# Optimization experiments

Measured on AMD Instinct MI355X. Metric: run time of the kernel, lower is better.

Reference implementation:

```python
import jax, jax.numpy as jnp
import numpy as np

GATE_SLOPE = 10.0
ALPHA = 0.8
STRIDE = 1
PADDING = 1


def _unfold(x, kH, kW, stride, padding):
    # torch F.unfold equivalent, kept as (B, Cin, kH, kW, Hout, Wout)
    B, C, H, W = x.shape
    xp = jnp.pad(x, ((0, 0), (0, 0), (padding, padding), (padding, padding)))
    Hout = (H + 2 * padding - kH) // stride + 1
    Wout = (W + 2 * padding - kW) // stride + 1
    cols = []
    for i in range(kH):          # small fixed loop over kernel taps (9 iters)
        for j in range(kW):
            cols.append(xp[:, :, i:i + Hout * stride:stride, j:j + Wout * stride:stride])
    return jnp.stack(cols, axis=2).reshape(B, C, kH, kW, Hout, Wout)


def setup_inputs() -> dict:
    key = jax.random.key(0)
    ks = jax.random.split(key, 6)
    B, Cin, H, W = 4, 16, 32, 32
    Cout, K, kH, kW = 32, 3, 3, 3
    pshape = (Cout, Cin, K, kH, kW)
    x = jax.random.normal(ks[0], (B, Cin, H, W), jnp.float32)
    k = jax.random.uniform(ks[1], pshape, jnp.float32) * 2.0 + 0.5
    Ec = jax.random.uniform(ks[2], pshape, jnp.float32) * 2.0 + 0.5
    Ps = jax.random.uniform(ks[3], pshape, jnp.float32) * 1.5 + 0.5
    bias = jax.random.normal(ks[4], pshape, jnp.float32) * 0.1
    coef = jax.random.normal(ks[5], pshape, jnp.float32)
    out_bias = jnp.zeros((Cout,), jnp.float32)
    return {"x": x, "k": k, "Ec": Ec, "Ps": Ps, "bias": bias, "coef": coef, "out_bias": out_bias}


def reference(x, k, Ec, Ps, bias, coef, out_bias):
    kH, kW = k.shape[-2], k.shape[-1]
    patches = _unfold(x, kH, kW, STRIDE, PADDING)          # (B,Cin,kH,kW,Hout,Wout)
    # broadcast layout: (B, Cout, Cin, K, kH, kW, Hout, Wout)
    xe = patches[:, None, :, None]                          # (B,1,Cin,1,kH,kW,Ho,Wo)
    def bc(p):
        return p[None, :, :, :, :, :, None, None]
    k_, Ec_, Ps_, b_, c_ = bc(k), bc(Ec), bc(Ps), bc(bias), bc(coef)
    # stateless mode: prev_x = detach(x_exp) -> dx == 0 in value, grad flows via xe
    prev_x = jax.lax.stop_gradient(xe)
    is_moving_up = jax.nn.sigmoid(GATE_SLOPE * (xe - prev_x))
    crossed_pos = jax.nn.sigmoid(GATE_SLOPE * (xe - Ec_))
    crossed_neg = jax.nn.sigmoid(GATE_SLOPE * (-xe - Ec_))
    su = is_moving_up * crossed_pos
    sl = (1.0 - is_moving_up) * crossed_neg
    # branch_prev = +1 (stateless)
    target_sign = su - sl + (1.0 - su - sl)
    branch_mom = ALPHA + (1.0 - ALPHA) * target_sign
    shifted_x = xe + Ec_ * branch_mom
    basis = Ps_ * jnp.tanh(k_ * shifted_x) + b_
    out = jnp.sum(basis * c_, axis=(2, 3, 4, 5))            # (B,Cout,Hout,Wout)
    return out + out_bias[None, :, None, None]
```

## Files before the change

kernel.cpp:

```cpp
#include <hip/hip_runtime.h>


#define LOG2E 1.4426950408889634f

__global__ __launch_bounds__(256, 8) void ferro_main(
    const float* __restrict__ x,
    const float* __restrict__ k, const float* __restrict__ Ec,
    const float* __restrict__ Ps, const float* __restrict__ bias,
    const float* __restrict__ coef, const float* __restrict__ out_bias,
    float* __restrict__ out)
{
    const int bid = blockIdx.x;
    const int rs  = bid & 15;
    const int co  = (bid >> 4) & 31;
    const int b   = bid >> 9;
    const int tid = threadIdx.x;

    __shared__ float4 p4s[432];
    __shared__ float  xs[16 * 4 * 34];
    __shared__ float  red[128];
    __shared__ float  redc[4];
    __shared__ float  csh;

    const int pbase = co * 432;
    float cpart = 0.f;
    for (int s = tid; s < 432; s += 256) {
        float kv = k[pbase + s];
        float ev = Ec[pbase + s];
        float pv = Ps[pbase + s];
        float bv = bias[pbase + s];
        float cv = coef[pbase + s];
        float G  = 2.f * LOG2E * kv;
        float4 v;
        v.x = ev;
        v.y = G;
        v.z = 0.1f * G * ev;
        v.w = -2.f * pv * cv;
        int cin = s / 27;
        int r   = s - cin * 27;
        int kk  = r / 9;
        int ij  = r - kk * 9;
        p4s[cin * 27 + ij * 3 + kk] = v;
        cpart += (pv + bv) * cv;
    }

    const int r0 = rs * 2;
    const float* xb = x + b * (16 * 1024);
    for (int idx = tid; idx < 16 * 136; idx += 256) {
        int cin  = idx / 136;
        int rem  = idx - cin * 136;
        int row4 = rem / 34;
        int colp = rem - row4 * 34;
        int gr = r0 + row4 - 1;
        int gc = colp - 1;
        float v = 0.f;
        if ((unsigned)gr < 32u && (unsigned)gc < 32u)
            v = xb[(cin * 32 + gr) * 32 + gc];
        xs[idx] = v;
    }

    #pragma unroll
    for (int off = 32; off > 0; off >>= 1)
        cpart += __shfl_down(cpart, off, 64);
    if ((tid & 63) == 0) redc[tid >> 6] = cpart;
    __syncthreads();
    if (tid == 0) csh = redc[0] + redc[1] + redc[2] + redc[3];
    __syncthreads();

    const int lane = tid & 63;
    const int w    = tid >> 6;
    const int row  = w >> 1;
    const int cinq = w & 1;
    const int col  = lane & 31;
    const int cinh = lane >> 5;
    float acc0 = 0.f, acc1 = 0.f, acc2 = 0.f;

    const int cinbase = cinq * 8 + cinh * 4;
    #pragma unroll 1
    for (int c = 0; c < 4; ++c) {
        const int cin = cinbase + c;
        const float*  xr = &xs[cin * 136 + row * 34 + col];
        const float4* pp = &p4s[cin * 27];
        #pragma unroll
        for (int ij = 0; ij < 9; ++ij) {
            const int i = ij / 3, j = ij - (ij / 3) * 3;
            float xv = xr[i * 34 + j];
            {
                float4 v = pp[ij * 3 + 0];
                float wv = xv + v.x;
                float q  = fmaf(wv, wv, 0.04f);
                float r  = __builtin_amdgcn_rsqf(q);
                float t  = fmaf(wv, r, -1.f);
                float a  = fmaf(v.z, t, v.y * wv);
                float e  = __builtin_amdgcn_exp2f(a);
                float u  = __builtin_amdgcn_rcpf(e + 1.f);
                acc0 = fmaf(v.w, u, acc0);
            }
            {
                float4 v = pp[ij * 3 + 1];
                float wv = xv + v.x;
                float q  = fmaf(wv, wv, 0.04f);
                float r  = __builtin_amdgcn_rsqf(q);
                float t  = fmaf(wv, r, -1.f);
                float a  = fmaf(v.z, t, v.y * wv);
                float e  = __builtin_amdgcn_exp2f(a);
                float u  = __builtin_amdgcn_rcpf(e + 1.f);
                acc1 = fmaf(v.w, u, acc1);
            }
            {
                float4 v = pp[ij * 3 + 2];
                float wv = xv + v.x;
                float q  = fmaf(wv, wv, 0.04f);
                float r  = __builtin_amdgcn_rsqf(q);
                float t  = fmaf(wv, r, -1.f);
                float a  = fmaf(v.z, t, v.y * wv);
                float e  = __builtin_amdgcn_exp2f(a);
                float u  = __builtin_amdgcn_rcpf(e + 1.f);
                acc2 = fmaf(v.w, u, acc2);
            }
        }
    }

    float acc = (acc0 + acc1) + acc2;
    acc += __shfl_xor(acc, 32, 64);
    if (cinh == 0) red[w * 32 + col] = acc;
    __syncthreads();

    if (tid < 64) {
        int r   = tid >> 5;
        int cl  = tid & 31;
        float v = red[(r * 2 + 0) * 32 + cl] + red[(r * 2 + 1) * 32 + cl]
                + csh + out_bias[co];
        out[((b * 32 + co) * 32 + (r0 + r)) * 32 + cl] = v;
    }
}

extern "C" void kernel_launch(void* const* d_in, const int* in_sizes, int n_in,
                              void* d_out, int out_size, void* d_ws, size_t ws_size,
                              hipStream_t stream) {
    const float* x        = (const float*)d_in[0];
    const float* k        = (const float*)d_in[1];
    const float* Ec       = (const float*)d_in[2];
    const float* Ps       = (const float*)d_in[3];
    const float* bias     = (const float*)d_in[4];
    const float* coef     = (const float*)d_in[5];
    const float* out_bias = (const float*)d_in[6];
    float* out = (float*)d_out;

    ferro_main<<<dim3(2048), dim3(256), 0, stream>>>(
        x, k, Ec, Ps, bias, coef, out_bias, out);
}
```

Measured before the change: 87.46 us.

## Split parameter prep into separate kernel and process four rows per block

Parameter preprocessing (the float4 packing and the constant bias term) moves into a small prep kernel that writes to workspace, so it is no longer repeated in every block of the main kernel. The main kernel then reads the parameters from global memory with wave-uniform indexing instead of from shared memory. Each block now covers four output rows instead of two, which halves the block count and reduces halo reloads of x. In exchange there is an extra kernel launch and a dependency between the two kernels, and the parameter reads now go through cache rather than LDS.

After: 91.42 us. 4.5% more time.

```diff
diff --git a/kernel.cpp b/kernel.cpp
--- a/kernel.cpp
+++ b/kernel.cpp
@@ -3,84 +3,95 @@
 
 #define LOG2E 1.4426950408889634f
 
-__global__ __launch_bounds__(256, 8) void ferro_main(
-    const float* __restrict__ x,
+__global__ __launch_bounds__(512) void ferro_prep(
     const float* __restrict__ k, const float* __restrict__ Ec,
     const float* __restrict__ Ps, const float* __restrict__ bias,
     const float* __restrict__ coef, const float* __restrict__ out_bias,
-    float* __restrict__ out)
+    float4* __restrict__ p4g, float* __restrict__ cg)
 {
-    const int bid = blockIdx.x;
-    const int rs  = bid & 15;
-    const int co  = (bid >> 4) & 31;
-    const int b   = bid >> 9;
+    const int co  = blockIdx.x;
     const int tid = threadIdx.x;
-
-    __shared__ float4 p4s[432];
-    __shared__ float  xs[16 * 4 * 34];
-    __shared__ float  red[128];
-    __shared__ float  redc[4];
-    __shared__ float  csh;
+    __shared__ float red[8];
 
     const int pbase = co * 432;
     float cpart = 0.f;
-    for (int s = tid; s < 432; s += 256) {
-        float kv = k[pbase + s];
-        float ev = Ec[pbase + s];
-        float pv = Ps[pbase + s];
-        float bv = bias[pbase + s];
-        float cv = coef[pbase + s];
+    if (tid < 432) {
+        float kv = k[pbase + tid];
+        float ev = Ec[pbase + tid];
+        float pv = Ps[pbase + tid];
+        float bv = bias[pbase + tid];
+        float cv = coef[pbase + tid];
         float G  = 2.f * LOG2E * kv;
         float4 v;
         v.x = ev;
         v.y = G;
         v.z = 0.1f * G * ev;
         v.w = -2.f * pv * cv;
-        int cin = s / 27;
-        int r   = s - cin * 27;
+        int cin = tid / 27;
+        int r   = tid - cin * 27;
         int kk  = r / 9;
         int ij  = r - kk * 9;
-        p4s[cin * 27 + ij * 3 + kk] = v;
-        cpart += (pv + bv) * cv;
+        p4g[pbase + cin * 27 + ij * 3 + kk] = v;
+        cpart = (pv + bv) * cv;
     }
+    #pragma unroll
+    for (int off = 32; off > 0; off >>= 1)
+        cpart += __shfl_down(cpart, off, 64);
+    if ((tid & 63) == 0) red[tid >> 6] = cpart;
+    __syncthreads();
+    if (tid == 0) {
+        float t = 0.f;
+        #pragma unroll
+        for (int w = 0; w < 8; ++w) t += red[w];
+        cg[co] = t + out_bias[co];
+    }
+}
 
-    const int r0 = rs * 2;
+__global__ __launch_bounds__(256, 4) void ferro_main(
+    const float* __restrict__ x,
+    const float4* __restrict__ p4g, const float* __restrict__ cg,
+    float* __restrict__ out)
+{
+    const int bid = blockIdx.x;
+    const int rq  = bid & 7;
+    const int co  = (bid >> 3) & 31;
+    const int b   = bid >> 8;
+    const int tid = threadIdx.x;
+
+    __shared__ float xs[16 * 6 * 34];
+    __shared__ float red[4 * 64];
+
+    const int r0 = rq * 4;
     const float* xb = x + b * (16 * 1024);
-    for (int idx = tid; idx < 16 * 136; idx += 256) {
-        int cin  = idx / 136;
-        int rem  = idx - cin * 136;
-        int row4 = rem / 34;
-        int colp = rem - row4 * 34;
-        int gr = r0 + row4 - 1;
+    for (int idx = tid; idx < 16 * 204; idx += 256) {
+        int cin  = idx / 204;
+        int rem  = idx - cin * 204;
+        int row6 = rem / 34;
+        int colp = rem - row6 * 34;
+        int gr = r0 + row6 - 1;
         int gc = colp - 1;
         float v = 0.f;
         if ((unsigned)gr < 32u && (unsigned)gc < 32u)
             v = xb[(cin * 32 + gr) * 32 + gc];
         xs[idx] = v;
     }
-
-    #pragma unroll
-    for (int off = 32; off > 0; off >>= 1)
-        cpart += __shfl_down(cpart, off, 64);
-    if ((tid & 63) == 0) redc[tid >> 6] = cpart;
-    __syncthreads();
-    if (tid == 0) csh = redc[0] + redc[1] + redc[2] + redc[3];
     __syncthreads();
 
+    const int wb   = __builtin_amdgcn_readfirstlane(tid) >> 6;
+    const int rp   = wb >> 1;
+    const int ch   = wb & 1;
     const int lane = tid & 63;
-    const int w    = tid >> 6;
-    const int row  = w >> 1;
-    const int cinq = w & 1;
+    const int prow = lane >> 5;
     const int col  = lane & 31;
-    const int cinh = lane >> 5;
+
+    const int lrbase = rp * 2 + prow;
     float acc0 = 0.f, acc1 = 0.f, acc2 = 0.f;
 
-    const int cinbase = cinq * 8 + cinh * 4;
     #pragma unroll 1
-    for (int c = 0; c < 4; ++c) {
-        const int cin = cinbase + c;
-        const float*  xr = &xs[cin * 136 + row * 34 + col];
-        const float4* pp = &p4s[cin * 27];
+    for (int c8 = 0; c8 < 8; ++c8) {
+        const int cin = ch * 8 + c8;
+        const float*  xr = &xs[cin * 204 + lrbase * 34 + col];
+        const float4* pp = &p4g[(co * 16 + cin) * 27];
         #pragma unroll
         for (int ij = 0; ij < 9; ++ij) {
             const int i = ij / 3, j = ij - (ij / 3) * 3;
@@ -121,17 +132,17 @@
         }
     }
 
-    float acc = (acc0 + acc1) + acc2;
-    acc += __shfl_xor(acc, 32, 64);
-    if (cinh == 0) red[w * 32 + col] = acc;
+    red[wb * 64 + lane] = (acc0 + acc1) + acc2;
     __syncthreads();
 
-    if (tid < 64) {
-        int r   = tid >> 5;
-        int cl  = tid & 31;
-        float v = red[(r * 2 + 0) * 32 + cl] + red[(r * 2 + 1) * 32 + cl]
-                + csh + out_bias[co];
-        out[((b * 32 + co) * 32 + (r0 + r)) * 32 + cl] = v;
+    if (tid < 128) {
+        int rp2 = tid >> 6;
+        int ln  = tid & 63;
+        float v = red[(rp2 * 2 + 0) * 64 + ln] + red[(rp2 * 2 + 1) * 64 + ln]
+                + cg[co];
+        int grow = r0 + rp2 * 2 + (ln >> 5);
+        int gcol = ln & 31;
+        out[((b * 32 + co) * 32 + grow) * 32 + gcol] = v;
     }
 }
 
@@ -147,6 +158,10 @@
     const float* out_bias = (const float*)d_in[6];
     float* out = (float*)d_out;
 
-    ferro_main<<<dim3(2048), dim3(256), 0, stream>>>(
-        x, k, Ec, Ps, bias, coef, out_bias, out);
+    float4* p4g = (float4*)d_ws;
+    float*  cg  = (float*)((char*)d_ws + 32 * 432 * 16);
+
+    ferro_prep<<<dim3(32), dim3(512), 0, stream>>>(
+        k, Ec, Ps, bias, coef, out_bias, p4g, cg);
+    ferro_main<<<dim3(1024), dim3(256), 0, stream>>>(x, p4g, cg, out);
 }
```
